# Kernel tuning notes

Measured on AMD Instinct MI355X. Metric: run time of the kernel, lower is better.

The kernel has to match this reference:

```python
import jax, jax.numpy as jnp
import numpy as np

OUTLINER_RATIO = 0.01
SUB_OUTLINER_BIT = 8


def _get_statistics(x, outliner_ratio, sub_bit):
    # threshold from the first batch element, as in torch.kthvalue(x[0].flatten(), ...)
    flat = jnp.abs(x[0]).ravel()
    k = int(flat.shape[0] * (1.0 - outliner_ratio))  # static python int
    outliner = jnp.sort(flat)[k - 1]
    x_out0 = jnp.where(jnp.abs(x[0]) > outliner, x[0], 0.0)
    x_sub0 = x[0] - x_out0
    qmax = float(2 ** (sub_bit - 1) - 1)
    scale = jnp.max(jnp.abs(x_sub0)) / qmax
    return outliner, scale


def _compress(x, outliner, scale, sub_bit):
    # split into fp outliers + low-bit quantized sub-outlier residual
    x_outlier = jnp.where(jnp.abs(x) > outliner, x, 0.0)
    x_sub = x - x_outlier
    qmin = -(2 ** (sub_bit - 1))
    qmax = 2 ** (sub_bit - 1) - 1
    q = jnp.clip(jnp.round(x_sub / scale), qmin, qmax).astype(jnp.int8)
    return x_outlier, q


def setup_inputs() -> dict:
    key = jax.random.key(0)
    x = jax.random.normal(key, (8, 2048, 4096), dtype=jnp.float32)
    return {"x": x}


def reference(x):
    # forward activation
    result = jax.nn.silu(x)
    # outlier-aware compression statistics (iteration < 10 path)
    outliner, scale = _get_statistics(x, OUTLINER_RATIO, SUB_OUTLINER_BIT)
    x_outlier_compressed, x_sub_q = _compress(x, outliner, scale, SUB_OUTLINER_BIT)
    # module returns (silu(x), outliner, max_norm_column_list, scale); the
    # column list is unused downstream so we return the float outputs
    return (result, outliner, scale)
```

## Files before the change

### kernel.cpp

```cpp
#include <hip/hip_runtime.h>

#define NBINS 4096
#define BPT (NBINS / 256)

struct SelState {
  unsigned prefix;
  unsigned krem;
  unsigned bins[NBINS];
};

__global__ __launch_bounds__(256) void init_state_kernel(SelState* st, unsigned k) {
  int t = threadIdx.x;
  for (int j = t; j < NBINS; j += 256) st->bins[j] = 0u;
  if (t == 0) { st->prefix = 0u; st->krem = k; }
}

__global__ __launch_bounds__(256) void silu_kernel(const float4* __restrict__ x,
                                                   float4* __restrict__ out, int nvec) {
  int i = blockIdx.x * blockDim.x + threadIdx.x;
  int stride = gridDim.x * blockDim.x;
  for (; i < nvec; i += stride) {
    float4 v = x[i];
    float4 r;
    r.x = v.x / (1.0f + __expf(-v.x));
    r.y = v.y / (1.0f + __expf(-v.y));
    r.z = v.z / (1.0f + __expf(-v.z));
    r.w = v.w / (1.0f + __expf(-v.w));
    out[i] = r;
  }
}

__global__ __launch_bounds__(256) void hist_kernel(const uint4* __restrict__ x, int nvec,
                                                   SelState* __restrict__ st,
                                                   unsigned shift, unsigned mask) {
  __shared__ unsigned lbins[NBINS];
  for (int j = threadIdx.x; j < NBINS; j += 256) lbins[j] = 0u;
  __syncthreads();
  unsigned prefix = st->prefix;
  int i = blockIdx.x * blockDim.x + threadIdx.x;
  int stride = gridDim.x * blockDim.x;
  for (; i < nvec; i += stride) {
    uint4 v = x[i];
    unsigned a;
    a = v.x & 0x7fffffffu; if ((a & mask) == prefix) atomicAdd(&lbins[(a >> shift) & (NBINS - 1)], 1u);
    a = v.y & 0x7fffffffu; if ((a & mask) == prefix) atomicAdd(&lbins[(a >> shift) & (NBINS - 1)], 1u);
    a = v.z & 0x7fffffffu; if ((a & mask) == prefix) atomicAdd(&lbins[(a >> shift) & (NBINS - 1)], 1u);
    a = v.w & 0x7fffffffu; if ((a & mask) == prefix) atomicAdd(&lbins[(a >> shift) & (NBINS - 1)], 1u);
  }
  __syncthreads();
  for (int j = threadIdx.x; j < NBINS; j += 256) {
    unsigned c = lbins[j];
    if (c) atomicAdd(&st->bins[j], c);
  }
}

__global__ __launch_bounds__(256) void scan_kernel(SelState* __restrict__ st, unsigned shift,
                                                   float* __restrict__ out_scalars) {
  __shared__ unsigned csum[256];
  const int t = threadIdx.x;
  unsigned local[BPT];
  unsigned s = 0;
  for (int j = 0; j < BPT; ++j) {
    local[j] = st->bins[t * BPT + j];
    s += local[j];
  }
  csum[t] = s;
  __syncthreads();
  for (int off = 1; off < 256; off <<= 1) {
    unsigned add = (t >= off) ? csum[t - off] : 0u;
    __syncthreads();
    csum[t] += add;
    __syncthreads();
  }
  unsigned incl = csum[t];
  unsigned excl = incl - s;
  unsigned krem = st->krem;
  if (krem > excl && krem <= incl) {
    unsigned run = excl;
    unsigned newprefix = st->prefix;
    for (int j = 0; j < BPT; ++j) {
      if (krem <= run + local[j]) {
        unsigned b = (unsigned)(t * BPT + j);
        newprefix |= (b << shift);
        st->prefix = newprefix;
        st->krem = krem - run;
        if (out_scalars) {
          float v = __uint_as_float(newprefix);
          out_scalars[0] = v;
          out_scalars[1] = v / 127.0f;
        }
        break;
      }
      run += local[j];
    }
  }
  __syncthreads();
  for (int j = 0; j < BPT; ++j) st->bins[t * BPT + j] = 0u;
}

extern "C" void kernel_launch(void* const* d_in, const int* in_sizes, int n_in,
                              void* d_out, int out_size, void* d_ws, size_t ws_size,
                              hipStream_t stream) {
  const float* x = (const float*)d_in[0];
  float* out = (float*)d_out;
  const int n = in_sizes[0];
  const int n0 = n / 8;
  const unsigned k = (unsigned)((double)n0 * 0.99);

  SelState* st = (SelState*)d_ws;

  init_state_kernel<<<1, 256, 0, stream>>>(st, k);

  const int nvec0 = n0 / 4;
  dim3 hb(256), hg(2048);
  hist_kernel<<<hg, hb, 0, stream>>>((const uint4*)x, nvec0, st, 19u, 0x00000000u);
  scan_kernel<<<1, 256, 0, stream>>>(st, 19u, nullptr);
  hist_kernel<<<hg, hb, 0, stream>>>((const uint4*)x, nvec0, st, 7u, 0xFFF80000u);
  scan_kernel<<<1, 256, 0, stream>>>(st, 7u, nullptr);
  hist_kernel<<<hg, hb, 0, stream>>>((const uint4*)x, nvec0, st, 0u, 0xFFFFFF80u);
  scan_kernel<<<1, 256, 0, stream>>>(st, 0u, out + n);

  const int nvec = n / 4;
  silu_kernel<<<4096, 256, 0, stream>>>((const float4*)x, (float4*)out, nvec);
}
```

Measured before the change: 513.5 us.

## Fuse first histogram pass into SiLU and compact candidates for final radix selection

```diff
diff --git a/kernel.cpp b/kernel.cpp
--- a/kernel.cpp
+++ b/kernel.cpp
@@ -1,69 +1,25 @@
 #include <hip/hip_runtime.h>
+
+typedef float vfloat4 __attribute__((ext_vector_type(4)));
 
 #define NBINS 4096
 #define BPT (NBINS / 256)
 
-struct SelState {
-  unsigned prefix;
-  unsigned krem;
-  unsigned bins[NBINS];
-};
-
-__global__ __launch_bounds__(256) void init_state_kernel(SelState* st, unsigned k) {
-  int t = threadIdx.x;
-  for (int j = t; j < NBINS; j += 256) st->bins[j] = 0u;
-  if (t == 0) { st->prefix = 0u; st->krem = k; }
-}
-
-__global__ __launch_bounds__(256) void silu_kernel(const float4* __restrict__ x,
-                                                   float4* __restrict__ out, int nvec) {
-  int i = blockIdx.x * blockDim.x + threadIdx.x;
-  int stride = gridDim.x * blockDim.x;
-  for (; i < nvec; i += stride) {
-    float4 v = x[i];
-    float4 r;
-    r.x = v.x / (1.0f + __expf(-v.x));
-    r.y = v.y / (1.0f + __expf(-v.y));
-    r.z = v.z / (1.0f + __expf(-v.z));
-    r.w = v.w / (1.0f + __expf(-v.w));
-    out[i] = r;
-  }
-}
-
-__global__ __launch_bounds__(256) void hist_kernel(const uint4* __restrict__ x, int nvec,
-                                                   SelState* __restrict__ st,
-                                                   unsigned shift, unsigned mask) {
-  __shared__ unsigned lbins[NBINS];
-  for (int j = threadIdx.x; j < NBINS; j += 256) lbins[j] = 0u;
-  __syncthreads();
-  unsigned prefix = st->prefix;
-  int i = blockIdx.x * blockDim.x + threadIdx.x;
-  int stride = gridDim.x * blockDim.x;
-  for (; i < nvec; i += stride) {
-    uint4 v = x[i];
-    unsigned a;
-    a = v.x & 0x7fffffffu; if ((a & mask) == prefix) atomicAdd(&lbins[(a >> shift) & (NBINS - 1)], 1u);
-    a = v.y & 0x7fffffffu; if ((a & mask) == prefix) atomicAdd(&lbins[(a >> shift) & (NBINS - 1)], 1u);
-    a = v.z & 0x7fffffffu; if ((a & mask) == prefix) atomicAdd(&lbins[(a >> shift) & (NBINS - 1)], 1u);
-    a = v.w & 0x7fffffffu; if ((a & mask) == prefix) atomicAdd(&lbins[(a >> shift) & (NBINS - 1)], 1u);
-  }
-  __syncthreads();
-  for (int j = threadIdx.x; j < NBINS; j += 256) {
-    unsigned c = lbins[j];
-    if (c) atomicAdd(&st->bins[j], c);
-  }
-}
-
-__global__ __launch_bounds__(256) void scan_kernel(SelState* __restrict__ st, unsigned shift,
-                                                   float* __restrict__ out_scalars) {
-  __shared__ unsigned csum[256];
+#define FUSED_BLOCKS   4096
+#define COMPACT_BLOCKS 2048
+
+#define OFF_COUNTER 0u
+#define OFF_BINS    256u
+#define OFF_SLICES  8192u
+
+__device__ __forceinline__ void select_bin(const unsigned* __restrict__ bins,
+                                           unsigned krem,
+                                           unsigned* csum, unsigned* res) {
   const int t = threadIdx.x;
   unsigned local[BPT];
   unsigned s = 0;
-  for (int j = 0; j < BPT; ++j) {
-    local[j] = st->bins[t * BPT + j];
-    s += local[j];
-  }
+#pragma unroll
+  for (int j = 0; j < BPT; ++j) { local[j] = bins[t * BPT + j]; s += local[j]; }
   csum[t] = s;
   __syncthreads();
   for (int off = 1; off < 256; off <<= 1) {
@@ -74,52 +30,182 @@
   }
   unsigned incl = csum[t];
   unsigned excl = incl - s;
-  unsigned krem = st->krem;
   if (krem > excl && krem <= incl) {
     unsigned run = excl;
-    unsigned newprefix = st->prefix;
+#pragma unroll
     for (int j = 0; j < BPT; ++j) {
       if (krem <= run + local[j]) {
-        unsigned b = (unsigned)(t * BPT + j);
-        newprefix |= (b << shift);
-        st->prefix = newprefix;
-        st->krem = krem - run;
-        if (out_scalars) {
-          float v = __uint_as_float(newprefix);
-          out_scalars[0] = v;
-          out_scalars[1] = v / 127.0f;
-        }
+        res[0] = (unsigned)(t * BPT + j);
+        res[1] = krem - run;
         break;
       }
       run += local[j];
     }
   }
   __syncthreads();
-  for (int j = 0; j < BPT; ++j) st->bins[t * BPT + j] = 0u;
+}
+
+__global__ __launch_bounds__(256) void fused_silu_hist(
+    const vfloat4* __restrict__ x, vfloat4* __restrict__ out,
+    int nvec, int nvec0, int vpb, unsigned* __restrict__ slices) {
+  __shared__ unsigned lbins[NBINS];
+  const int b = blockIdx.x;
+  const int start = b * vpb;
+  const int end = min(start + vpb, nvec);
+  const bool do_hist = (start < nvec0);
+
+  if (do_hist) {
+    for (int j = threadIdx.x; j < NBINS; j += 256) lbins[j] = 0u;
+    __syncthreads();
+    for (int i = start + (int)threadIdx.x; i < end; i += 256) {
+      vfloat4 v = x[i];
+      if (i < nvec0) {
+        unsigned a;
+        a = __float_as_uint(v.x) & 0x7fffffffu; atomicAdd(&lbins[a >> 19], 1u);
+        a = __float_as_uint(v.y) & 0x7fffffffu; atomicAdd(&lbins[a >> 19], 1u);
+        a = __float_as_uint(v.z) & 0x7fffffffu; atomicAdd(&lbins[a >> 19], 1u);
+        a = __float_as_uint(v.w) & 0x7fffffffu; atomicAdd(&lbins[a >> 19], 1u);
+      }
+      vfloat4 r;
+      r.x = v.x / (1.0f + __expf(-v.x));
+      r.y = v.y / (1.0f + __expf(-v.y));
+      r.z = v.z / (1.0f + __expf(-v.z));
+      r.w = v.w / (1.0f + __expf(-v.w));
+      __builtin_nontemporal_store(r, &out[i]);
+    }
+    __syncthreads();
+    unsigned* slice = slices + (size_t)b * NBINS;
+    for (int j = threadIdx.x; j < NBINS; j += 256) slice[j] = lbins[j];
+  } else {
+    for (int i = start + (int)threadIdx.x; i < end; i += 256) {
+      vfloat4 v = x[i];
+      vfloat4 r;
+      r.x = v.x / (1.0f + __expf(-v.x));
+      r.y = v.y / (1.0f + __expf(-v.y));
+      r.z = v.z / (1.0f + __expf(-v.z));
+      r.w = v.w / (1.0f + __expf(-v.w));
+      __builtin_nontemporal_store(r, &out[i]);
+    }
+  }
+}
+
+__global__ __launch_bounds__(256) void reduce_hist(
+    const unsigned* __restrict__ slices, unsigned* __restrict__ bins,
+    unsigned* __restrict__ counter, int hist_blocks) {
+  const int j = blockIdx.x * 256 + threadIdx.x;
+  unsigned s = 0;
+  for (int b = 0; b < hist_blocks; ++b) s += slices[(size_t)b * NBINS + j];
+  bins[j] = s;
+  if (j == 0) *counter = 0u;
+}
+
+__global__ __launch_bounds__(256) void compact_kernel(
+    const uint4* __restrict__ x, int nvec0, int vpb,
+    const unsigned* __restrict__ bins, unsigned* __restrict__ counter,
+    unsigned* __restrict__ cand, unsigned krem) {
+  __shared__ unsigned csum[256];
+  __shared__ unsigned res[2];
+  select_bin(bins, krem, csum, res);
+  const unsigned prefix12 = res[0];
+
+  const int start = blockIdx.x * vpb;
+  const int end = min(start + vpb, nvec0);
+  const int lane = (int)(threadIdx.x & 63u);
+  for (int i = start + (int)threadIdx.x; i < end; i += 256) {
+    uint4 v = x[i];
+    unsigned aa[4] = { v.x & 0x7fffffffu, v.y & 0x7fffffffu,
+                       v.z & 0x7fffffffu, v.w & 0x7fffffffu };
+#pragma unroll
+    for (int c = 0; c < 4; ++c) {
+      const unsigned abs_ = aa[c];
+      const bool m = ((abs_ >> 19) == prefix12);
+      const unsigned long long mk = __ballot(m);
+      if (mk) {
+        const int leader = __ffsll((long long)mk) - 1;
+        unsigned base = 0;
+        if (lane == leader) base = atomicAdd(counter, (unsigned)__popcll(mk));
+        base = __shfl(base, leader);
+        if (m) {
+          const unsigned pos =
+              (unsigned)__popcll(mk & ((1ull << (unsigned)lane) - 1ull));
+          cand[base + pos] = abs_;
+        }
+      }
+    }
+  }
+}
+
+__global__ __launch_bounds__(256) void final_select_kernel(
+    const unsigned* __restrict__ bins, const unsigned* __restrict__ counter,
+    const unsigned* __restrict__ cand, unsigned krem,
+    float* __restrict__ out_scalars) {
+  __shared__ unsigned lbins[NBINS];
+  __shared__ unsigned csum[256];
+  __shared__ unsigned res[2];
+  const int t = threadIdx.x;
+
+  select_bin(bins, krem, csum, res);
+  const unsigned prefix12 = res[0];
+  const unsigned krem2 = res[1];
+  __syncthreads();
+  const unsigned nc = *counter;
+
+  for (int j = t; j < NBINS; j += 256) lbins[j] = 0u;
+  __syncthreads();
+  for (unsigned i = (unsigned)t; i < nc; i += 256)
+    atomicAdd(&lbins[(cand[i] >> 7) & 0xfffu], 1u);
+  __syncthreads();
+  select_bin(lbins, krem2, csum, res);
+  const unsigned b2 = res[0];
+  const unsigned krem3 = res[1];
+  __syncthreads();
+
+  for (int j = t; j < NBINS; j += 256) lbins[j] = 0u;
+  __syncthreads();
+  const unsigned pref24 = (prefix12 << 12) | b2;
+  for (unsigned i = (unsigned)t; i < nc; i += 256) {
+    const unsigned a = cand[i];
+    if ((a >> 7) == pref24) atomicAdd(&lbins[a & 0x7fu], 1u);
+  }
+  __syncthreads();
+  select_bin(lbins, krem3, csum, res);
+  const unsigned b3 = res[0];
+
+  if (t == 0) {
+    const unsigned pattern = (pref24 << 7) | b3;
+    const float v = __uint_as_float(pattern);
+    out_scalars[0] = v;
+    out_scalars[1] = v / 127.0f;
+  }
 }
 
 extern "C" void kernel_launch(void* const* d_in, const int* in_sizes, int n_in,
-                              void* d_out, int out_size, void* d_ws, size_t ws_size,
-                              hipStream_t stream) {
+                              void* d_out, int out_size, void* d_ws,
+                              size_t ws_size, hipStream_t stream) {
   const float* x = (const float*)d_in[0];
   float* out = (float*)d_out;
   const int n = in_sizes[0];
   const int n0 = n / 8;
   const unsigned k = (unsigned)((double)n0 * 0.99);
 
-  SelState* st = (SelState*)d_ws;
-
-  init_state_kernel<<<1, 256, 0, stream>>>(st, k);
-
+  const int nvec  = n / 4;
   const int nvec0 = n0 / 4;
-  dim3 hb(256), hg(2048);
-  hist_kernel<<<hg, hb, 0, stream>>>((const uint4*)x, nvec0, st, 19u, 0x00000000u);
-  scan_kernel<<<1, 256, 0, stream>>>(st, 19u, nullptr);
-  hist_kernel<<<hg, hb, 0, stream>>>((const uint4*)x, nvec0, st, 7u, 0xFFF80000u);
-  scan_kernel<<<1, 256, 0, stream>>>(st, 7u, nullptr);
-  hist_kernel<<<hg, hb, 0, stream>>>((const uint4*)x, nvec0, st, 0u, 0xFFFFFF80u);
-  scan_kernel<<<1, 256, 0, stream>>>(st, 0u, out + n);
-
-  const int nvec = n / 4;
-  silu_kernel<<<4096, 256, 0, stream>>>((const float4*)x, (float4*)out, nvec);
-}
+
+  unsigned* ws32    = (unsigned*)d_ws;
+  unsigned* counter = ws32 + OFF_COUNTER;
+  unsigned* bins    = ws32 + OFF_BINS;
+  unsigned* slices  = ws32 + OFF_SLICES;
+
+  const int vpb_f = (nvec + FUSED_BLOCKS - 1) / FUSED_BLOCKS;
+  const int hist_blocks = (nvec0 + vpb_f - 1) / vpb_f;
+  unsigned* cand = slices + (size_t)hist_blocks * NBINS;
+  const int vpb_c = (nvec0 + COMPACT_BLOCKS - 1) / COMPACT_BLOCKS;
+
+  fused_silu_hist<<<FUSED_BLOCKS, 256, 0, stream>>>(
+      (const vfloat4*)x, (vfloat4*)out, nvec, nvec0, vpb_f, slices);
+  reduce_hist<<<NBINS / 256, 256, 0, stream>>>(slices, bins, counter,
+                                               hist_blocks);
+  compact_kernel<<<COMPACT_BLOCKS, 256, 0, stream>>>(
+      (const uint4*)x, nvec0, vpb_c, bins, counter, cand, k);
+  final_select_kernel<<<1, 256, 0, stream>>>(bins, counter, cand, k, out + n);
+}
```

New measurement: 896.7 us. +74.6%, slower.
